# Kernel optimization log

Measured on AMD Instinct MI355X. Metric: run time of the kernel, lower is better.

## Reference

```python
import jax, jax.numpy as jnp
import numpy as np

NUM_EMBEDDINGS = 1024
EMBEDDING_DIM = 256
COMMITMENT_COST = 0.25


def setup_inputs() -> dict:
    key = jax.random.key(0)
    k1, k2 = jax.random.split(key)
    z_e = jax.random.normal(k1, (32, 256, 32, 32), dtype=jnp.float32)
    # nn.init.uniform_(weight, -1/K, 1/K)
    bound = 1.0 / NUM_EMBEDDINGS
    weight = jax.random.uniform(k2, (NUM_EMBEDDINGS, EMBEDDING_DIM), dtype=jnp.float32,
                                minval=-bound, maxval=bound)
    return {"z_e": z_e, "weight": weight}


def reference(z_e, weight):
    B, C, H, W = z_e.shape
    sg = jax.lax.stop_gradient
    # (B, H, W, C) -> (N, C)
    flat = jnp.transpose(z_e, (0, 2, 3, 1)).reshape(-1, C)
    # squared L2 distances to each codebook vector: (N, K)
    dist = (jnp.sum(flat * flat, axis=1, keepdims=True)
            - 2.0 * flat @ weight.T
            + jnp.sum(weight * weight, axis=1))
    indices = jnp.argmin(dist, axis=1)  # (N,)
    # codebook lookup (equivalent to one-hot @ weight)
    quantized = weight[indices].reshape(B, H, W, C)
    quantized = jnp.transpose(quantized, (0, 3, 1, 2))  # (B, C, H, W)
    e_latent = jnp.mean((sg(quantized) - z_e) ** 2)
    q_latent = jnp.mean((quantized - sg(z_e)) ** 2)
    loss = q_latent + COMMITMENT_COST * e_latent
    # straight-through estimator
    quantized_st = z_e + sg(quantized - z_e)
    # codebook usage perplexity: avg_probs = mean of one-hot encodings
    n = flat.shape[0]
    counts = jax.ops.segment_sum(jnp.ones((n,), dtype=z_e.dtype), indices,
                                 num_segments=NUM_EMBEDDINGS)
    avg_probs = counts / n
    perplexity = jnp.exp(-jnp.sum(avg_probs * jnp.log(avg_probs + 1e-10)))
    return (quantized_st, loss, perplexity)
```

## Files before the change

### kernel.cpp

```cpp
#include <hip/hip_runtime.h>
#include <float.h>
#include <math.h>
#include <stdint.h>


#define NB   32
#define NC   256
#define NHW  1024
#define NK   1024
#define NELEM (NB*NC*NHW)

typedef __attribute__((ext_vector_type(8))) short bf16x8;
typedef __attribute__((ext_vector_type(4))) float f32x4;

__device__ __forceinline__ unsigned short f2bf(float f) {
    unsigned u = __float_as_uint(f);
    u += 0x7FFFu + ((u >> 16) & 1u);
    return (unsigned short)(u >> 16);
}

__global__ __launch_bounds__(256) void vq_wsq(const float* __restrict__ w,
                                              float* __restrict__ wsq) {
    const int lane = threadIdx.x & 63;
    const int wave = threadIdx.x >> 6;
    const int k = blockIdx.x * 4 + wave;
    const float* row = w + k * NC;
    float s = 0.f;
#pragma unroll
    for (int p = 0; p < 4; ++p) {
        float v = row[lane + p * 64];
        s = fmaf(v, v, s);
    }
#pragma unroll
    for (int off = 32; off; off >>= 1) s += __shfl_down(s, off, 64);
    if (lane == 0) wsq[k] = s;
}

__global__ __launch_bounds__(256) void vq_pack(const float* __restrict__ w,
                                               unsigned short* __restrict__ cb) {
    const int t = blockIdx.x;
#pragma unroll
    for (int rep = 0; rep < 2; ++rep) {
        const int p = threadIdx.x + rep * 256;
        const int cc = p >> 6, l = p & 63;
        const int n = l & 15, quad = l >> 4;
        const float* src = w + (t * 16 + n) * NC + cc * 32 + quad * 8;
        const float4 f0 = *(const float4*)src;
        const float4 f1 = *(const float4*)(src + 4);
        union { unsigned short u[8]; uint4 v; } pk;
        pk.u[0] = f2bf(-2.f * f0.x); pk.u[1] = f2bf(-2.f * f0.y);
        pk.u[2] = f2bf(-2.f * f0.z); pk.u[3] = f2bf(-2.f * f0.w);
        pk.u[4] = f2bf(-2.f * f1.x); pk.u[5] = f2bf(-2.f * f1.y);
        pk.u[6] = f2bf(-2.f * f1.z); pk.u[7] = f2bf(-2.f * f1.w);
        *(uint4*)(cb + (size_t)t * 4096 + cc * 512 + l * 8) = pk.v;
    }
}

__global__ __launch_bounds__(512) void vq_main2(const float* __restrict__ z,
                                                const float* __restrict__ w,
                                                const float* __restrict__ wsq,
                                                const unsigned short* __restrict__ cb,
                                                unsigned int* __restrict__ counts,
                                                float* __restrict__ loss_sum,
                                                float* __restrict__ out) {
    __shared__ __align__(16) char cbuf[2][32768];
    int*   fidx = (int*)cbuf[0];
    float* lred = (float*)(cbuf[0] + 1024);

    const int tid  = threadIdx.x;
    const int wv   = tid >> 6;
    const int lane = tid & 63;
    const int n    = lane & 15;
    const int quad = lane >> 4;
    const int bid  = blockIdx.x;
    const int b    = bid >> 3;
    const int hw0  = (bid & 7) << 7;
    const int hwb  = hw0 + wv * 16;

    const float* zb = z + (size_t)b * (NC * NHW);

    bf16x8 bfr[8];
#pragma unroll
    for (int cc = 0; cc < 8; ++cc) {
        const float* zp = zb + (size_t)(cc * 32 + quad * 8) * NHW + hwb + n;
        union { unsigned short u[8]; bf16x8 v; } pk;
#pragma unroll
        for (int j = 0; j < 8; ++j) pk.u[j] = f2bf(zp[(size_t)j * NHW]);
        bfr[cc] = pk.v;
    }

    const char* cbb = (const char*)cb;
#define STAGE(ch)                                                              \
    {                                                                          \
        const char* gsrc = cbb + (size_t)(ch) * 32768 + wv * 4096 + lane * 16; \
        char* ldst = cbuf[(ch) & 1] + wv * 4096;                               \
        _Pragma("unroll")                                                      \
        for (int i = 0; i < 4; ++i) {                                          \
            __builtin_amdgcn_global_load_lds(                                  \
                (const __attribute__((address_space(1))) unsigned int*)        \
                    (uintptr_t)(gsrc + i * 1024),                              \
                (__attribute__((address_space(3))) unsigned int*)              \
                    (uint32_t)(uintptr_t)(ldst + i * 1024),                    \
                16, 0, 0);                                                     \
        }                                                                      \
    }

    float bestv = FLT_MAX;
    int   besti = 0;

    STAGE(0);
    for (int ch = 0; ch < 16; ++ch) {
        __syncthreads();
        if (ch + 1 < 16) STAGE(ch + 1);
        const char* bufc = cbuf[ch & 1];
#pragma unroll
        for (int tp = 0; tp < 2; ++tp) {
            const int tt0 = tp * 2, tt1 = tp * 2 + 1;
            const int kt0 = (ch * 4 + tt0) * 16;
            const int kt1 = kt0 + 16;
            f32x4 acc0 = *(const f32x4*)(wsq + kt0 + quad * 4);
            f32x4 acc1 = *(const f32x4*)(wsq + kt1 + quad * 4);
#pragma unroll
            for (int cc = 0; cc < 8; ++cc) {
                bf16x8 a0 = *(const bf16x8*)(bufc + (tt0 * 8 + cc) * 1024 + lane * 16);
                bf16x8 a1 = *(const bf16x8*)(bufc + (tt1 * 8 + cc) * 1024 + lane * 16);
                acc0 = __builtin_amdgcn_mfma_f32_16x16x32_bf16(a0, bfr[cc], acc0, 0, 0, 0);
                acc1 = __builtin_amdgcn_mfma_f32_16x16x32_bf16(a1, bfr[cc], acc1, 0, 0, 0);
            }
#pragma unroll
            for (int r = 0; r < 4; ++r) {
                const float v0 = acc0[r];
                if (v0 < bestv) { bestv = v0; besti = kt0 + quad * 4 + r; }
                const float v1 = acc1[r];
                if (v1 < bestv) { bestv = v1; besti = kt1 + quad * 4 + r; }
            }
        }
    }

#pragma unroll
    for (int off = 16; off <= 32; off <<= 1) {
        const float ov = __shfl_xor(bestv, off, 64);
        const int   ok = __shfl_xor(besti, off, 64);
        if (ov < bestv || (ov == bestv && ok < besti)) { bestv = ov; besti = ok; }
    }
    __syncthreads();
    if (lane < 16) fidx[wv * 16 + lane] = besti;
    __syncthreads();
    if (tid < 128) atomicAdd(&counts[fidx[tid]], 1u);

    float lsum = 0.f;
    const int hwl = tid & 127;
    const int cg  = tid >> 7;
    const int myk = fidx[hwl];
    const float* wr  = w + myk * NC;
    const float* zp2 = zb + hw0 + hwl;
    float*       op  = out + (size_t)b * (NC * NHW) + hw0 + hwl;
#pragma unroll 4
    for (int p = 0; p < 16; ++p) {
        const int c0 = cg * 64 + p * 4;
        const float4 q4 = *(const float4*)(wr + c0);
        const float qa[4] = {q4.x, q4.y, q4.z, q4.w};
#pragma unroll
        for (int u = 0; u < 4; ++u) {
            const int c = c0 + u;
            const float zv = zp2[(size_t)c * NHW];
            const float d = qa[u] - zv;
            lsum = fmaf(d, d, lsum);
            op[(size_t)c * NHW] = qa[u];
        }
    }
#pragma unroll
    for (int off = 32; off; off >>= 1) lsum += __shfl_down(lsum, off, 64);
    if (lane == 0) lred[wv] = lsum;
    __syncthreads();
    if (tid == 0) {
        float t = 0.f;
#pragma unroll
        for (int i = 0; i < 8; ++i) t += lred[i];
        atomicAdd(loss_sum, t);
    }
}

__global__ __launch_bounds__(256) void vq_final(const unsigned int* __restrict__ counts,
                                                const float* __restrict__ loss_sum,
                                                float* __restrict__ out) {
    __shared__ float red[4];
    const int tid = threadIdx.x;
    float s = 0.f;
#pragma unroll
    for (int p = 0; p < 4; ++p) {
        const float pr = (float)counts[tid + p * 256] * (1.f / 32768.f);
        s = fmaf(pr, logf(pr + 1e-10f), s);
    }
#pragma unroll
    for (int off = 32; off; off >>= 1) s += __shfl_down(s, off, 64);
    if ((tid & 63) == 0) red[tid >> 6] = s;
    __syncthreads();
    if (tid == 0) {
        const float tot = red[0] + red[1] + red[2] + red[3];
        out[NELEM]     = loss_sum[0] * (1.25f / (float)NELEM);
        out[NELEM + 1] = expf(-tot);
    }
}

extern "C" void kernel_launch(void* const* d_in, const int* in_sizes, int n_in,
                              void* d_out, int out_size, void* d_ws, size_t ws_size,
                              hipStream_t stream) {
    const float* z = (const float*)d_in[0];
    const float* w = (const float*)d_in[1];
    float* out = (float*)d_out;

    float*          wsq      = (float*)d_ws;
    unsigned int*   counts   = (unsigned int*)((char*)d_ws + 4096);
    float*          loss_sum = (float*)((char*)d_ws + 8192);
    unsigned short* cbfrag   = (unsigned short*)((char*)d_ws + 16384);

    hipMemsetAsync((char*)d_ws + 4096, 0, 4100, stream);

    vq_wsq  <<<256, 256, 0, stream>>>(w, wsq);
    vq_pack <<<64,  256, 0, stream>>>(w, cbfrag);
    vq_main2<<<256, 512, 0, stream>>>(z, w, wsq, cbfrag, counts, loss_sum, out);
    vq_final<<<1,   256, 0, stream>>>(counts, loss_sum, out);
}
```

Before: 130.7 us.

## Fuse prep kernels, split codebook across waves, fold finalization into main kernel

Merges the codebook-norm and bf16-packing kernels plus the counter memset into a single prep kernel. The final perplexity/loss kernel is folded into the main kernel using a last-block-done atomic counter. The main kernel now runs 512 blocks of 256 threads, each covering 64 positions. Each wave handles 32 positions against half the codebook, and the two halves are merged through LDS. This removes launches and memsets and doubles the B-fragment reuse per A load, at the cost of extra cross-wave reduction and an atomic completion protocol.

```diff
diff --git a/kernel.cpp b/kernel.cpp
--- a/kernel.cpp
+++ b/kernel.cpp
@@ -9,6 +9,7 @@
 #define NHW  1024
 #define NK   1024
 #define NELEM (NB*NC*NHW)
+#define GRID_MAIN 512
 
 typedef __attribute__((ext_vector_type(8))) short bf16x8;
 typedef __attribute__((ext_vector_type(4))) float f32x4;
@@ -19,29 +20,26 @@
     return (unsigned short)(u >> 16);
 }
 
-__global__ __launch_bounds__(256) void vq_wsq(const float* __restrict__ w,
-                                              float* __restrict__ wsq) {
-    const int lane = threadIdx.x & 63;
-    const int wave = threadIdx.x >> 6;
-    const int k = blockIdx.x * 4 + wave;
-    const float* row = w + k * NC;
-    float s = 0.f;
-#pragma unroll
-    for (int p = 0; p < 4; ++p) {
-        float v = row[lane + p * 64];
-        s = fmaf(v, v, s);
-    }
-#pragma unroll
-    for (int off = 32; off; off >>= 1) s += __shfl_down(s, off, 64);
-    if (lane == 0) wsq[k] = s;
-}
-
-__global__ __launch_bounds__(256) void vq_pack(const float* __restrict__ w,
-                                               unsigned short* __restrict__ cb) {
-    const int t = blockIdx.x;
-#pragma unroll
-    for (int rep = 0; rep < 2; ++rep) {
-        const int p = threadIdx.x + rep * 256;
+__global__ __launch_bounds__(256) void vq_prep(const float* __restrict__ w,
+                                               float* __restrict__ wsq,
+                                               unsigned short* __restrict__ cb,
+                                               unsigned int* __restrict__ counts,
+                                               unsigned int* __restrict__ lossdone) {
+    const int tid = threadIdx.x, b = blockIdx.x;
+    const int lane = tid & 63, wv = tid >> 6;
+    {
+        const int k = b * 4 + wv;
+        const float* row = w + k * NC;
+        float s = 0.f;
+#pragma unroll
+        for (int p = 0; p < 4; ++p) { float v = row[lane + p * 64]; s = fmaf(v, v, s); }
+#pragma unroll
+        for (int off = 32; off; off >>= 1) s += __shfl_down(s, off, 64);
+        if (lane == 0) wsq[k] = s;
+    }
+    const int gt = b * 256 + tid;
+    if (gt < 32768) {
+        const int t = gt >> 9, p = gt & 511;
         const int cc = p >> 6, l = p & 63;
         const int n = l & 15, quad = l >> 4;
         const float* src = w + (t * 16 + n) * NC + cc * 32 + quad * 8;
@@ -52,109 +50,143 @@
         pk.u[2] = f2bf(-2.f * f0.z); pk.u[3] = f2bf(-2.f * f0.w);
         pk.u[4] = f2bf(-2.f * f1.x); pk.u[5] = f2bf(-2.f * f1.y);
         pk.u[6] = f2bf(-2.f * f1.z); pk.u[7] = f2bf(-2.f * f1.w);
-        *(uint4*)(cb + (size_t)t * 4096 + cc * 512 + l * 8) = pk.v;
-    }
-}
-
-__global__ __launch_bounds__(512) void vq_main2(const float* __restrict__ z,
+        *(uint4*)(cb + (size_t)t * 4096 + cc * 512 + (size_t)l * 8) = pk.v;
+    }
+    if (b == 128) {
+#pragma unroll
+        for (int i = 0; i < 4; ++i) counts[tid * 4 + i] = 0u;
+        if (tid < 2) lossdone[tid] = 0u;
+    }
+}
+
+__global__ __launch_bounds__(256) void vq_main3(const float* __restrict__ z,
                                                 const float* __restrict__ w,
                                                 const float* __restrict__ wsq,
                                                 const unsigned short* __restrict__ cb,
                                                 unsigned int* __restrict__ counts,
-                                                float* __restrict__ loss_sum,
+                                                unsigned int* __restrict__ lossdone,
                                                 float* __restrict__ out) {
     __shared__ __align__(16) char cbuf[2][32768];
-    int*   fidx = (int*)cbuf[0];
-    float* lred = (float*)(cbuf[0] + 1024);
+    int*   fidx  = (int*)(cbuf[0]);
+    float* pscr  = (float*)(cbuf[0] + 256);
+    int*   pidx  = (int*)(cbuf[0] + 768);
+    float* lred  = (float*)(cbuf[0] + 1280);
+    int*   lflag = (int*)(cbuf[0] + 1296);
+    float* red2  = (float*)(cbuf[0] + 1312);
 
     const int tid  = threadIdx.x;
-    const int wv   = tid >> 6;
-    const int lane = tid & 63;
-    const int n    = lane & 15;
-    const int quad = lane >> 4;
-    const int bid  = blockIdx.x;
-    const int b    = bid >> 3;
-    const int hw0  = (bid & 7) << 7;
-    const int hwb  = hw0 + wv * 16;
-
-    const float* zb = z + (size_t)b * (NC * NHW);
-
-    bf16x8 bfr[8];
-#pragma unroll
-    for (int cc = 0; cc < 8; ++cc) {
-        const float* zp = zb + (size_t)(cc * 32 + quad * 8) * NHW + hwb + n;
-        union { unsigned short u[8]; bf16x8 v; } pk;
-#pragma unroll
-        for (int j = 0; j < 8; ++j) pk.u[j] = f2bf(zp[(size_t)j * NHW]);
-        bfr[cc] = pk.v;
-    }
-
+    const int wv   = tid >> 6, lane = tid & 63;
+    const int n    = lane & 15, quad = lane >> 4;
+    const int zhalf = wv & 1;
+    const int chalf = wv >> 1;
+    const int b   = blockIdx.x;
+    const int img = b >> 4;
+    const int hw0 = (b & 15) << 6;
+    const float* zb = z + (size_t)img * (NC * NHW);
     const char* cbb = (const char*)cb;
+
 #define STAGE(ch)                                                              \
     {                                                                          \
-        const char* gsrc = cbb + (size_t)(ch) * 32768 + wv * 4096 + lane * 16; \
-        char* ldst = cbuf[(ch) & 1] + wv * 4096;                               \
         _Pragma("unroll")                                                      \
-        for (int i = 0; i < 4; ++i) {                                          \
+        for (int i = 0; i < 8; ++i) {                                          \
+            const int q = i >> 1, part = i & 1;                                \
+            const int tq = (q >> 1) * 32 + (ch) * 2 + (q & 1);                 \
+            const char* gsrc = cbb + (size_t)tq * 8192 + part * 4096 + tid * 16;\
+            char* ldst = cbuf[(ch) & 1] + i * 4096 + tid * 16;                 \
             __builtin_amdgcn_global_load_lds(                                  \
                 (const __attribute__((address_space(1))) unsigned int*)        \
-                    (uintptr_t)(gsrc + i * 1024),                              \
+                    (uintptr_t)gsrc,                                           \
                 (__attribute__((address_space(3))) unsigned int*)              \
-                    (uint32_t)(uintptr_t)(ldst + i * 1024),                    \
+                    (uint32_t)(uintptr_t)ldst,                                 \
                 16, 0, 0);                                                     \
         }                                                                      \
     }
 
-    float bestv = FLT_MAX;
-    int   besti = 0;
-
     STAGE(0);
+
+    bf16x8 bfr[2][8];
+#pragma unroll
+    for (int s = 0; s < 2; ++s) {
+#pragma unroll
+        for (int cc = 0; cc < 8; ++cc) {
+            const float* zp = zb + (size_t)(cc * 32 + quad * 8) * NHW
+                              + hw0 + zhalf * 32 + s * 16 + n;
+            union { unsigned short u[8]; bf16x8 v; } pk;
+#pragma unroll
+            for (int j = 0; j < 8; ++j) pk.u[j] = f2bf(zp[(size_t)j * NHW]);
+            bfr[s][cc] = pk.v;
+        }
+    }
+
+    float bestv[2] = {FLT_MAX, FLT_MAX};
+    int   besti[2] = {0, 0};
+
     for (int ch = 0; ch < 16; ++ch) {
         __syncthreads();
         if (ch + 1 < 16) STAGE(ch + 1);
         const char* bufc = cbuf[ch & 1];
-#pragma unroll
-        for (int tp = 0; tp < 2; ++tp) {
-            const int tt0 = tp * 2, tt1 = tp * 2 + 1;
-            const int kt0 = (ch * 4 + tt0) * 16;
-            const int kt1 = kt0 + 16;
-            f32x4 acc0 = *(const f32x4*)(wsq + kt0 + quad * 4);
-            f32x4 acc1 = *(const f32x4*)(wsq + kt1 + quad * 4);
-#pragma unroll
-            for (int cc = 0; cc < 8; ++cc) {
-                bf16x8 a0 = *(const bf16x8*)(bufc + (tt0 * 8 + cc) * 1024 + lane * 16);
-                bf16x8 a1 = *(const bf16x8*)(bufc + (tt1 * 8 + cc) * 1024 + lane * 16);
-                acc0 = __builtin_amdgcn_mfma_f32_16x16x32_bf16(a0, bfr[cc], acc0, 0, 0, 0);
-                acc1 = __builtin_amdgcn_mfma_f32_16x16x32_bf16(a1, bfr[cc], acc1, 0, 0, 0);
-            }
-#pragma unroll
-            for (int r = 0; r < 4; ++r) {
-                const float v0 = acc0[r];
-                if (v0 < bestv) { bestv = v0; besti = kt0 + quad * 4 + r; }
-                const float v1 = acc1[r];
-                if (v1 < bestv) { bestv = v1; besti = kt1 + quad * 4 + r; }
-            }
-        }
-    }
-
-#pragma unroll
-    for (int off = 16; off <= 32; off <<= 1) {
-        const float ov = __shfl_xor(bestv, off, 64);
-        const int   ok = __shfl_xor(besti, off, 64);
-        if (ov < bestv || (ov == bestv && ok < besti)) { bestv = ov; besti = ok; }
-    }
-    __syncthreads();
-    if (lane < 16) fidx[wv * 16 + lane] = besti;
-    __syncthreads();
-    if (tid < 128) atomicAdd(&counts[fidx[tid]], 1u);
+        const int kt0 = (chalf * 32 + ch * 2) * 16;
+        const int kt1 = kt0 + 16;
+        const int slot0 = chalf * 2, slot1 = slot0 + 1;
+        f32x4 acc00 = *(const f32x4*)(wsq + kt0 + quad * 4);
+        f32x4 acc01 = acc00;
+        f32x4 acc10 = *(const f32x4*)(wsq + kt1 + quad * 4);
+        f32x4 acc11 = acc10;
+#pragma unroll
+        for (int cc = 0; cc < 8; ++cc) {
+            const bf16x8 a0 = *(const bf16x8*)(bufc + slot0 * 8192 + cc * 1024 + lane * 16);
+            const bf16x8 a1 = *(const bf16x8*)(bufc + slot1 * 8192 + cc * 1024 + lane * 16);
+            acc00 = __builtin_amdgcn_mfma_f32_16x16x32_bf16(a0, bfr[0][cc], acc00, 0, 0, 0);
+            acc01 = __builtin_amdgcn_mfma_f32_16x16x32_bf16(a0, bfr[1][cc], acc01, 0, 0, 0);
+            acc10 = __builtin_amdgcn_mfma_f32_16x16x32_bf16(a1, bfr[0][cc], acc10, 0, 0, 0);
+            acc11 = __builtin_amdgcn_mfma_f32_16x16x32_bf16(a1, bfr[1][cc], acc11, 0, 0, 0);
+        }
+#pragma unroll
+        for (int r = 0; r < 4; ++r) {
+            const int k0 = kt0 + quad * 4 + r, k1 = kt1 + quad * 4 + r;
+            if (acc00[r] < bestv[0]) { bestv[0] = acc00[r]; besti[0] = k0; }
+            if (acc01[r] < bestv[1]) { bestv[1] = acc01[r]; besti[1] = k0; }
+            if (acc10[r] < bestv[0]) { bestv[0] = acc10[r]; besti[0] = k1; }
+            if (acc11[r] < bestv[1]) { bestv[1] = acc11[r]; besti[1] = k1; }
+        }
+    }
+
+#pragma unroll
+    for (int s = 0; s < 2; ++s) {
+        float bv = bestv[s]; int bi = besti[s];
+#pragma unroll
+        for (int off = 16; off <= 32; off <<= 1) {
+            const float ov = __shfl_xor(bv, off, 64);
+            const int   ok = __shfl_xor(bi, off, 64);
+            if (ov < bv || (ov == bv && ok < bi)) { bv = ov; bi = ok; }
+        }
+        bestv[s] = bv; besti[s] = bi;
+    }
+    __syncthreads();
+    if (lane < 16) {
+#pragma unroll
+        for (int s = 0; s < 2; ++s) {
+            const int zloc = zhalf * 32 + s * 16 + lane;
+            pscr[chalf * 64 + zloc] = bestv[s];
+            pidx[chalf * 64 + zloc] = besti[s];
+        }
+    }
+    __syncthreads();
+    if (tid < 64) {
+        const float s0 = pscr[tid], s1 = pscr[64 + tid];
+        const int bi = (s1 < s0) ? pidx[64 + tid] : pidx[tid];
+        fidx[tid] = bi;
+        atomicAdd(&counts[bi], 1u);
+    }
+    __syncthreads();
 
     float lsum = 0.f;
-    const int hwl = tid & 127;
-    const int cg  = tid >> 7;
+    const int hwl = tid & 63;
+    const int cg  = tid >> 6;
     const int myk = fidx[hwl];
     const float* wr  = w + myk * NC;
     const float* zp2 = zb + hw0 + hwl;
-    float*       op  = out + (size_t)b * (NC * NHW) + hw0 + hwl;
+    float*       op  = out + (size_t)img * (NC * NHW) + hw0 + hwl;
 #pragma unroll 4
     for (int p = 0; p < 16; ++p) {
         const int c0 = cg * 64 + p * 4;
@@ -174,32 +206,32 @@
     if (lane == 0) lred[wv] = lsum;
     __syncthreads();
     if (tid == 0) {
-        float t = 0.f;
-#pragma unroll
-        for (int i = 0; i < 8; ++i) t += lred[i];
-        atomicAdd(loss_sum, t);
-    }
-}
-
-__global__ __launch_bounds__(256) void vq_final(const unsigned int* __restrict__ counts,
-                                                const float* __restrict__ loss_sum,
-                                                float* __restrict__ out) {
-    __shared__ float red[4];
-    const int tid = threadIdx.x;
-    float s = 0.f;
-#pragma unroll
-    for (int p = 0; p < 4; ++p) {
-        const float pr = (float)counts[tid + p * 256] * (1.f / 32768.f);
-        s = fmaf(pr, logf(pr + 1e-10f), s);
-    }
-#pragma unroll
-    for (int off = 32; off; off >>= 1) s += __shfl_down(s, off, 64);
-    if ((tid & 63) == 0) red[tid >> 6] = s;
-    __syncthreads();
-    if (tid == 0) {
-        const float tot = red[0] + red[1] + red[2] + red[3];
-        out[NELEM]     = loss_sum[0] * (1.25f / (float)NELEM);
-        out[NELEM + 1] = expf(-tot);
+        atomicAdd((float*)lossdone, lred[0] + lred[1] + lred[2] + lred[3]);
+        const unsigned old = __hip_atomic_fetch_add(&lossdone[1], 1u,
+                                 __ATOMIC_ACQ_REL, __HIP_MEMORY_SCOPE_AGENT);
+        lflag[0] = (old == GRID_MAIN - 1) ? 1 : 0;
+    }
+    __syncthreads();
+    if (lflag[0]) {
+        float s = 0.f;
+#pragma unroll
+        for (int p = 0; p < 4; ++p) {
+            const unsigned c = __hip_atomic_load(&counts[tid + p * 256],
+                                   __ATOMIC_RELAXED, __HIP_MEMORY_SCOPE_AGENT);
+            const float pr = (float)c * (1.f / 32768.f);
+            s = fmaf(pr, logf(pr + 1e-10f), s);
+        }
+#pragma unroll
+        for (int off = 32; off; off >>= 1) s += __shfl_down(s, off, 64);
+        if (lane == 0) red2[wv] = s;
+        __syncthreads();
+        if (tid == 0) {
+            const float tot = red2[0] + red2[1] + red2[2] + red2[3];
+            const float ls = __hip_atomic_load((float*)lossdone,
+                                 __ATOMIC_RELAXED, __HIP_MEMORY_SCOPE_AGENT);
+            out[NELEM]     = ls * (1.25f / (float)NELEM);
+            out[NELEM + 1] = expf(-tot);
+        }
     }
 }
 
@@ -212,13 +244,9 @@
 
     float*          wsq      = (float*)d_ws;
     unsigned int*   counts   = (unsigned int*)((char*)d_ws + 4096);
-    float*          loss_sum = (float*)((char*)d_ws + 8192);
+    unsigned int*   lossdone = (unsigned int*)((char*)d_ws + 8192);
     unsigned short* cbfrag   = (unsigned short*)((char*)d_ws + 16384);
 
-    hipMemsetAsync((char*)d_ws + 4096, 0, 4100, stream);
-
-    vq_wsq  <<<256, 256, 0, stream>>>(w, wsq);
-    vq_pack <<<64,  256, 0, stream>>>(w, cbfrag);
-    vq_main2<<<256, 512, 0, stream>>>(z, w, wsq, cbfrag, counts, loss_sum, out);
-    vq_final<<<1,   256, 0, stream>>>(counts, loss_sum, out);
-}
+    vq_prep <<<256,       256, 0, stream>>>(w, wsq, cbfrag, counts, lossdone);
+    vq_main3<<<GRID_MAIN, 256, 0, stream>>>(z, w, wsq, cbfrag, counts, lossdone, out);
+}
```

Measured after the change: 136.3 us. 4.3% more time.
